# Kernel tuning notes

Measured on AMD Instinct MI355X. Metric: run time of the kernel, lower is better.

The kernel has to match this reference:

```python
import jax, jax.numpy as jnp
import numpy as np

B, D, K, N = 32, 512, 64, 1024
EPS = 1e-12  # torch F.normalize eps


def setup_inputs() -> dict:
    key = jax.random.key(0)
    k1, k2, k3 = jax.random.split(key, 3)
    x = jax.random.normal(k1, (B, D, N), dtype=jnp.float32)
    conv_w = jax.random.normal(k2, (K, D), dtype=jnp.float32) * (1.0 / np.sqrt(D))
    centers = jax.random.normal(k3, (D, K), dtype=jnp.float32)
    return {"x": x, "conv_w": conv_w, "centers": centers}


def reference(x, conv_w, centers):
    # scores: 1x1 conv over flattened spatial dim -> [B, K, N]
    scores = jnp.einsum('kd,bdn->bkn', conv_w, x)
    assign = jax.nn.softmax(scores, axis=1)                 # softmax over clusters
    # Algebraic rewrite of sum_n assign[b,k,n] * (x[b,d,n] - centers[d,k]):
    vlad = (jnp.einsum('bdn,bkn->bdk', x, assign)
            - centers[None, :, :] * assign.sum(axis=-1)[:, None, :])  # [B, D, K]
    # intra-normalization over descriptor dim D (F.normalize with eps clamp)
    vlad = vlad / jnp.maximum(jnp.linalg.norm(vlad, axis=1, keepdims=True), EPS)
    desc = vlad.reshape(vlad.shape[0], -1)                  # [B, D*K]
    desc = desc / jnp.maximum(jnp.linalg.norm(desc, axis=1, keepdims=True), EPS)
    return desc
```

## Files before the change

kernel.cpp:

```cpp
#include <hip/hip_runtime.h>
#include <hip/hip_bf16.h>

#define Bv 32
#define Dv 512
#define Kv 64
#define Nv 1024
#define EPSv 1e-12f

typedef __attribute__((ext_vector_type(8))) short bf16x8;
typedef __attribute__((ext_vector_type(4))) float f32x4;

__device__ __forceinline__ unsigned short f2b(float f) {
  union { float f; unsigned u; } v; v.f = f;
  unsigned r = v.u + 0x7fffu + ((v.u >> 16) & 1u);
  return (unsigned short)(r >> 16);
}
__device__ __forceinline__ unsigned pack2(float a, float b) {
  return (unsigned)f2b(a) | ((unsigned)f2b(b) << 16);
}

__global__ __launch_bounds__(256) void wconv(const float* __restrict__ w,
                                             unsigned short* __restrict__ wbf) {
  int i = (blockIdx.x * 256 + threadIdx.x) * 4;
  float4 v = *(const float4*)&w[i];
  uint2 o = make_uint2(pack2(v.x, v.y), pack2(v.z, v.w));
  *(uint2*)&wbf[i] = o;
}

__global__ __launch_bounds__(512) void fused_scores(
    const float* __restrict__ x, const unsigned short* __restrict__ wbf,
    unsigned short* __restrict__ xbf, unsigned short* __restrict__ assign,
    float* __restrict__ asum) {
  __shared__ unsigned short xT[64 * 520];
  __shared__ float redmax[4][64];
  __shared__ float redsum[4][64];

  const int t = threadIdx.x;
  const int b = blockIdx.y;
  const int n0 = blockIdx.x * 64;

  {
    const int lo = t & 15;
    const int hi = t >> 4;
    const float* xb = x + (size_t)b * Dv * Nv + n0;
    unsigned short* xo = xbf + (size_t)b * Dv * Nv + n0;
#pragma unroll
    for (int r = 0; r < 8; r++) {
      int d = (hi + 32 * r) * 2;
      int n4 = lo * 4;
      float4 v0 = *(const float4*)&xb[(size_t)d * Nv + n4];
      float4 v1 = *(const float4*)&xb[(size_t)(d + 1) * Nv + n4];
      *(uint2*)&xo[(size_t)d * Nv + n4] =
          make_uint2(pack2(v0.x, v0.y), pack2(v0.z, v0.w));
      *(uint2*)&xo[(size_t)(d + 1) * Nv + n4] =
          make_uint2(pack2(v1.x, v1.y), pack2(v1.z, v1.w));
      *(unsigned*)&xT[(n4 + 0) * 520 + d] = pack2(v0.x, v1.x);
      *(unsigned*)&xT[(n4 + 1) * 520 + d] = pack2(v0.y, v1.y);
      *(unsigned*)&xT[(n4 + 2) * 520 + d] = pack2(v0.z, v1.z);
      *(unsigned*)&xT[(n4 + 3) * 520 + d] = pack2(v0.w, v1.w);
    }
  }
  __syncthreads();

  const int wv = t >> 6;
  const int lane = t & 63;
  const int q = lane >> 4;
  const int m = lane & 15;
  const int k16 = wv & 3;
  const int nsub = wv >> 2;

  f32x4 acc0 = {0.f, 0.f, 0.f, 0.f};
  f32x4 acc1 = {0.f, 0.f, 0.f, 0.f};

  const unsigned short* wp = wbf + (size_t)(k16 * 16 + m) * Dv + q * 8;
  const unsigned short* l0 = &xT[(nsub * 32 + m) * 520 + q * 8];
  const unsigned short* l1 = l0 + 16 * 520;

#pragma unroll
  for (int d0 = 0; d0 < Dv; d0 += 32) {
    bf16x8 af = *(const bf16x8*)(wp + d0);
    bf16x8 bf0 = *(const bf16x8*)(l0 + d0);
    bf16x8 bf1 = *(const bf16x8*)(l1 + d0);
    acc0 = __builtin_amdgcn_mfma_f32_16x16x32_bf16(af, bf0, acc0, 0, 0, 0);
    acc1 = __builtin_amdgcn_mfma_f32_16x16x32_bf16(af, bf1, acc1, 0, 0, 0);
  }

  float m0 = fmaxf(fmaxf(acc0[0], acc0[1]), fmaxf(acc0[2], acc0[3]));
  float m1 = fmaxf(fmaxf(acc1[0], acc1[1]), fmaxf(acc1[2], acc1[3]));
  m0 = fmaxf(m0, __shfl_xor(m0, 16)); m0 = fmaxf(m0, __shfl_xor(m0, 32));
  m1 = fmaxf(m1, __shfl_xor(m1, 16)); m1 = fmaxf(m1, __shfl_xor(m1, 32));
  if (q == 0) {
    redmax[k16][nsub * 32 + m] = m0;
    redmax[k16][nsub * 32 + 16 + m] = m1;
  }
  __syncthreads();
  const int c0 = nsub * 32 + m, c1 = c0 + 16;
  float mc0 = fmaxf(fmaxf(redmax[0][c0], redmax[1][c0]), fmaxf(redmax[2][c0], redmax[3][c0]));
  float mc1 = fmaxf(fmaxf(redmax[0][c1], redmax[1][c1]), fmaxf(redmax[2][c1], redmax[3][c1]));

  float e0[4], e1[4];
  float s0 = 0.f, s1 = 0.f;
#pragma unroll
  for (int r = 0; r < 4; r++) {
    e0[r] = __expf(acc0[r] - mc0); s0 += e0[r];
    e1[r] = __expf(acc1[r] - mc1); s1 += e1[r];
  }
  s0 += __shfl_xor(s0, 16); s0 += __shfl_xor(s0, 32);
  s1 += __shfl_xor(s1, 16); s1 += __shfl_xor(s1, 32);
  if (q == 0) {
    redsum[k16][c0] = s0;
    redsum[k16][c1] = s1;
  }
  __syncthreads();
  float sc0 = 1.0f / (redsum[0][c0] + redsum[1][c0] + redsum[2][c0] + redsum[3][c0]);
  float sc1 = 1.0f / (redsum[0][c1] + redsum[1][c1] + redsum[2][c1] + redsum[3][c1]);

  unsigned short* ab = assign + ((size_t)b * Kv + k16 * 16 + q * 4) * Nv + n0 + nsub * 32;
#pragma unroll
  for (int r = 0; r < 4; r++) {
    float v0 = e0[r] * sc0;
    float v1 = e1[r] * sc1;
    ab[(size_t)r * Nv + m] = f2b(v0);
    ab[(size_t)r * Nv + 16 + m] = f2b(v1);
    float p = v0 + v1;
    p += __shfl_xor(p, 1); p += __shfl_xor(p, 2);
    p += __shfl_xor(p, 4); p += __shfl_xor(p, 8);
    if (m == 0) atomicAdd(&asum[b * Kv + k16 * 16 + q * 4 + r], p);
  }
}

__global__ __launch_bounds__(512, 4) void vlad_mfma(
    const unsigned short* __restrict__ xbf, const unsigned short* __restrict__ assign,
    const float* __restrict__ centers, const float* __restrict__ asum,
    float* __restrict__ vlad, float* __restrict__ colsq) {
  __shared__ float sred[4][64][4];

  const int t = threadIdx.x;
  const int b = blockIdx.y;
  const int d0 = blockIdx.x * 16;
  const int wv = t >> 6;
  const int ksub = wv & 3;
  const int nh = wv >> 2;
  const int lane = t & 63;
  const int q = lane >> 4;
  const int m = lane & 15;
  const int k16 = ksub * 16;

  const unsigned short* xp = xbf + ((size_t)b * Dv + d0 + m) * Nv + nh * 512 + q * 8;
  const unsigned short* ap = assign + ((size_t)b * Kv + k16 + m) * Nv + nh * 512 + q * 8;

  f32x4 acc = {0.f, 0.f, 0.f, 0.f};
  bf16x8 xv[8], av[8];
#pragma unroll
  for (int i = 0; i < 8; i++) {
    xv[i] = *(const bf16x8*)(xp + i * 32);
    av[i] = *(const bf16x8*)(ap + i * 32);
  }
#pragma unroll
  for (int i = 0; i < 8; i++) {
    acc = __builtin_amdgcn_mfma_f32_16x16x32_bf16(xv[i], av[i], acc, 0, 0, 0);
    xv[i] = *(const bf16x8*)(xp + 256 + i * 32);
    av[i] = *(const bf16x8*)(ap + 256 + i * 32);
  }
#pragma unroll
  for (int i = 0; i < 8; i++)
    acc = __builtin_amdgcn_mfma_f32_16x16x32_bf16(xv[i], av[i], acc, 0, 0, 0);

  if (nh == 1) {
#pragma unroll
    for (int r = 0; r < 4; r++) sred[ksub][lane][r] = acc[r];
  }
  __syncthreads();
  if (nh == 0) {
    const int k = k16 + m;
    const float as = asum[b * Kv + k];
    float ss = 0.f;
#pragma unroll
    for (int r = 0; r < 4; r++) {
      float v = acc[r] + sred[ksub][lane][r];
      int d = d0 + q * 4 + r;
      float val = v - centers[d * Kv + k] * as;
      vlad[((size_t)b * Dv + d) * Kv + k] = val;
      ss = fmaf(val, val, ss);
    }
    ss += __shfl_xor(ss, 16);
    ss += __shfl_xor(ss, 32);
    if (q == 0) atomicAdd(&colsq[b * Kv + k], ss);
  }
}

__global__ __launch_bounds__(256) void scale_kernel(
    const float* __restrict__ vlad, const float* __restrict__ colsq,
    float* __restrict__ out) {
  const int t = threadIdx.x;
  const size_t i = (size_t)blockIdx.x * 256 + t;
  const int b = (int)(i >> 15);
  __shared__ float scs[64];
  __shared__ float bsh;
  if (t < 64) {
    float tot = colsq[b * Kv + t];
    float sc = 1.0f / fmaxf(sqrtf(tot), EPSv);
    scs[t] = sc;
    float contrib = tot * sc * sc;
#pragma unroll
    for (int off = 32; off > 0; off >>= 1) contrib += __shfl_down(contrib, off);
    if (t == 0) bsh = 1.0f / fmaxf(sqrtf(contrib), EPSv);
  }
  __syncthreads();
  out[i] = vlad[i] * scs[i & 63] * bsh;
}

extern "C" void kernel_launch(void* const* d_in, const int* in_sizes, int n_in,
                              void* d_out, int out_size, void* d_ws, size_t ws_size,
                              hipStream_t stream) {
  const float* x = (const float*)d_in[0];
  const float* w = (const float*)d_in[1];
  const float* centers = (const float*)d_in[2];
  float* out = (float*)d_out;

  char* ws = (char*)d_ws;
  unsigned short* assign = (unsigned short*)ws;
  float* vlad = (float*)(ws + 4194304);
  unsigned short* xbf = (unsigned short*)(ws + 8388608);
  unsigned short* wbf = (unsigned short*)(ws + 41943040);
  float* asum = (float*)(ws + 42008576);
  float* colsq = asum + Bv * Kv;

  hipMemsetAsync(asum, 0, (size_t)2 * Bv * Kv * sizeof(float), stream);

  wconv<<<32, 256, 0, stream>>>(w, wbf);
  fused_scores<<<dim3(Nv / 64, Bv), 512, 0, stream>>>(x, wbf, xbf, assign, asum);
  vlad_mfma<<<dim3(Dv / 16, Bv), 512, 0, stream>>>(xbf, assign, centers, asum, vlad, colsq);
  scale_kernel<<<(Bv * Dv * Kv) / 256, 256, 0, stream>>>(vlad, colsq, out);
}
```

Before: 147.2 us.

## Drop bf16 copy of x; convert fp32 x inline in vlad GEMM

```diff
diff --git a/kernel.cpp b/kernel.cpp
--- a/kernel.cpp
+++ b/kernel.cpp
@@ -29,8 +29,7 @@
 
 __global__ __launch_bounds__(512) void fused_scores(
     const float* __restrict__ x, const unsigned short* __restrict__ wbf,
-    unsigned short* __restrict__ xbf, unsigned short* __restrict__ assign,
-    float* __restrict__ asum) {
+    unsigned short* __restrict__ assign, float* __restrict__ asum) {
   __shared__ unsigned short xT[64 * 520];
   __shared__ float redmax[4][64];
   __shared__ float redsum[4][64];
@@ -42,22 +41,26 @@
   {
     const int lo = t & 15;
     const int hi = t >> 4;
+    const int s = (lo >> 1) & 3;
     const float* xb = x + (size_t)b * Dv * Nv + n0;
-    unsigned short* xo = xbf + (size_t)b * Dv * Nv + n0;
 #pragma unroll
     for (int r = 0; r < 8; r++) {
       int d = (hi + 32 * r) * 2;
       int n4 = lo * 4;
       float4 v0 = *(const float4*)&xb[(size_t)d * Nv + n4];
       float4 v1 = *(const float4*)&xb[(size_t)(d + 1) * Nv + n4];
-      *(uint2*)&xo[(size_t)d * Nv + n4] =
-          make_uint2(pack2(v0.x, v0.y), pack2(v0.z, v0.w));
-      *(uint2*)&xo[(size_t)(d + 1) * Nv + n4] =
-          make_uint2(pack2(v1.x, v1.y), pack2(v1.z, v1.w));
-      *(unsigned*)&xT[(n4 + 0) * 520 + d] = pack2(v0.x, v1.x);
-      *(unsigned*)&xT[(n4 + 1) * 520 + d] = pack2(v0.y, v1.y);
-      *(unsigned*)&xT[(n4 + 2) * 520 + d] = pack2(v0.z, v1.z);
-      *(unsigned*)&xT[(n4 + 3) * 520 + d] = pack2(v0.w, v1.w);
+      unsigned w0 = pack2(v0.x, v1.x);
+      unsigned w1 = pack2(v0.y, v1.y);
+      unsigned w2 = pack2(v0.z, v1.z);
+      unsigned w3 = pack2(v0.w, v1.w);
+      unsigned a0 = (s & 1) ? w1 : w0, a1 = (s & 1) ? w2 : w1,
+               a2 = (s & 1) ? w3 : w2, a3 = (s & 1) ? w0 : w3;
+      unsigned b0 = (s & 2) ? a2 : a0, b1 = (s & 2) ? a3 : a1,
+               b2 = (s & 2) ? a0 : a2, b3 = (s & 2) ? a1 : a3;
+      *(unsigned*)&xT[(n4 + ((0 + s) & 3)) * 520 + d] = b0;
+      *(unsigned*)&xT[(n4 + ((1 + s) & 3)) * 520 + d] = b1;
+      *(unsigned*)&xT[(n4 + ((2 + s) & 3)) * 520 + d] = b2;
+      *(unsigned*)&xT[(n4 + ((3 + s) & 3)) * 520 + d] = b3;
     }
   }
   __syncthreads();
@@ -129,64 +132,50 @@
   }
 }
 
-__global__ __launch_bounds__(512, 4) void vlad_mfma(
-    const unsigned short* __restrict__ xbf, const unsigned short* __restrict__ assign,
+__global__ __launch_bounds__(256, 4) void vlad_mfma(
+    const float* __restrict__ x, const unsigned short* __restrict__ assign,
     const float* __restrict__ centers, const float* __restrict__ asum,
     float* __restrict__ vlad, float* __restrict__ colsq) {
-  __shared__ float sred[4][64][4];
-
   const int t = threadIdx.x;
   const int b = blockIdx.y;
   const int d0 = blockIdx.x * 16;
-  const int wv = t >> 6;
-  const int ksub = wv & 3;
-  const int nh = wv >> 2;
+  const int ksub = t >> 6;
   const int lane = t & 63;
   const int q = lane >> 4;
   const int m = lane & 15;
   const int k16 = ksub * 16;
 
-  const unsigned short* xp = xbf + ((size_t)b * Dv + d0 + m) * Nv + nh * 512 + q * 8;
-  const unsigned short* ap = assign + ((size_t)b * Kv + k16 + m) * Nv + nh * 512 + q * 8;
+  const float* xp = x + ((size_t)b * Dv + d0 + m) * Nv + q * 8;
+  const unsigned short* ap = assign + ((size_t)b * Kv + k16 + m) * Nv + q * 8;
 
   f32x4 acc = {0.f, 0.f, 0.f, 0.f};
-  bf16x8 xv[8], av[8];
-#pragma unroll
-  for (int i = 0; i < 8; i++) {
-    xv[i] = *(const bf16x8*)(xp + i * 32);
-    av[i] = *(const bf16x8*)(ap + i * 32);
-  }
-#pragma unroll
-  for (int i = 0; i < 8; i++) {
-    acc = __builtin_amdgcn_mfma_f32_16x16x32_bf16(xv[i], av[i], acc, 0, 0, 0);
-    xv[i] = *(const bf16x8*)(xp + 256 + i * 32);
-    av[i] = *(const bf16x8*)(ap + 256 + i * 32);
-  }
-#pragma unroll
-  for (int i = 0; i < 8; i++)
-    acc = __builtin_amdgcn_mfma_f32_16x16x32_bf16(xv[i], av[i], acc, 0, 0, 0);
-
-  if (nh == 1) {
-#pragma unroll
-    for (int r = 0; r < 4; r++) sred[ksub][lane][r] = acc[r];
-  }
-  __syncthreads();
-  if (nh == 0) {
-    const int k = k16 + m;
-    const float as = asum[b * Kv + k];
-    float ss = 0.f;
-#pragma unroll
-    for (int r = 0; r < 4; r++) {
-      float v = acc[r] + sred[ksub][lane][r];
-      int d = d0 + q * 4 + r;
-      float val = v - centers[d * Kv + k] * as;
-      vlad[((size_t)b * Dv + d) * Kv + k] = val;
-      ss = fmaf(val, val, ss);
-    }
-    ss += __shfl_xor(ss, 16);
-    ss += __shfl_xor(ss, 32);
-    if (q == 0) atomicAdd(&colsq[b * Kv + k], ss);
-  }
+#pragma unroll
+  for (int n = 0; n < Nv; n += 32) {
+    float4 f0 = *(const float4*)(xp + n);
+    float4 f1 = *(const float4*)(xp + n + 4);
+    bf16x8 av = *(const bf16x8*)(ap + n);
+    bf16x8 xv;
+    unsigned* xu = (unsigned*)&xv;
+    xu[0] = pack2(f0.x, f0.y);
+    xu[1] = pack2(f0.z, f0.w);
+    xu[2] = pack2(f1.x, f1.y);
+    xu[3] = pack2(f1.z, f1.w);
+    acc = __builtin_amdgcn_mfma_f32_16x16x32_bf16(xv, av, acc, 0, 0, 0);
+  }
+
+  const int k = k16 + m;
+  const float as = asum[b * Kv + k];
+  float ss = 0.f;
+#pragma unroll
+  for (int r = 0; r < 4; r++) {
+    int d = d0 + q * 4 + r;
+    float val = acc[r] - centers[d * Kv + k] * as;
+    vlad[((size_t)b * Dv + d) * Kv + k] = val;
+    ss = fmaf(val, val, ss);
+  }
+  ss += __shfl_xor(ss, 16);
+  ss += __shfl_xor(ss, 32);
+  if (q == 0) atomicAdd(&colsq[b * Kv + k], ss);
 }
 
 __global__ __launch_bounds__(256) void scale_kernel(
@@ -221,15 +210,14 @@
   char* ws = (char*)d_ws;
   unsigned short* assign = (unsigned short*)ws;
   float* vlad = (float*)(ws + 4194304);
-  unsigned short* xbf = (unsigned short*)(ws + 8388608);
-  unsigned short* wbf = (unsigned short*)(ws + 41943040);
-  float* asum = (float*)(ws + 42008576);
+  unsigned short* wbf = (unsigned short*)(ws + 8388608);
+  float* asum = (float*)(ws + 8454144);
   float* colsq = asum + Bv * Kv;
 
   hipMemsetAsync(asum, 0, (size_t)2 * Bv * Kv * sizeof(float), stream);
 
   wconv<<<32, 256, 0, stream>>>(w, wbf);
-  fused_scores<<<dim3(Nv / 64, Bv), 512, 0, stream>>>(x, wbf, xbf, assign, asum);
-  vlad_mfma<<<dim3(Dv / 16, Bv), 512, 0, stream>>>(xbf, assign, centers, asum, vlad, colsq);
+  fused_scores<<<dim3(Nv / 64, Bv), 512, 0, stream>>>(x, wbf, assign, asum);
+  vlad_mfma<<<dim3(Dv / 16, Bv), 256, 0, stream>>>(x, assign, centers, asum, vlad, colsq);
   scale_kernel<<<(Bv * Dv * Kv) / 256, 256, 0, stream>>>(vlad, colsq, out);
 }
```

New measurement: 154.8 us. 5.2% more time.

## Tile xbf and assign by 64-column blocks and swizzle LDS transpose writes

Applied to the files above, without the earlier changes.

```diff
diff --git a/kernel.cpp b/kernel.cpp
--- a/kernel.cpp
+++ b/kernel.cpp
@@ -37,27 +37,37 @@
 
   const int t = threadIdx.x;
   const int b = blockIdx.y;
-  const int n0 = blockIdx.x * 64;
+  const int nt = blockIdx.x;
+  const int n0 = nt * 64;
 
   {
     const int lo = t & 15;
     const int hi = t >> 4;
+    const int s = (lo >> 1) & 3;
     const float* xb = x + (size_t)b * Dv * Nv + n0;
-    unsigned short* xo = xbf + (size_t)b * Dv * Nv + n0;
+    unsigned short* xt = xbf + ((size_t)b * 16 + nt) * (Dv * 64);
 #pragma unroll
     for (int r = 0; r < 8; r++) {
       int d = (hi + 32 * r) * 2;
       int n4 = lo * 4;
       float4 v0 = *(const float4*)&xb[(size_t)d * Nv + n4];
       float4 v1 = *(const float4*)&xb[(size_t)(d + 1) * Nv + n4];
-      *(uint2*)&xo[(size_t)d * Nv + n4] =
+      *(uint2*)&xt[(size_t)d * 64 + n4] =
           make_uint2(pack2(v0.x, v0.y), pack2(v0.z, v0.w));
-      *(uint2*)&xo[(size_t)(d + 1) * Nv + n4] =
+      *(uint2*)&xt[(size_t)(d + 1) * 64 + n4] =
           make_uint2(pack2(v1.x, v1.y), pack2(v1.z, v1.w));
-      *(unsigned*)&xT[(n4 + 0) * 520 + d] = pack2(v0.x, v1.x);
-      *(unsigned*)&xT[(n4 + 1) * 520 + d] = pack2(v0.y, v1.y);
-      *(unsigned*)&xT[(n4 + 2) * 520 + d] = pack2(v0.z, v1.z);
-      *(unsigned*)&xT[(n4 + 3) * 520 + d] = pack2(v0.w, v1.w);
+      unsigned w0 = pack2(v0.x, v1.x);
+      unsigned w1 = pack2(v0.y, v1.y);
+      unsigned w2 = pack2(v0.z, v1.z);
+      unsigned w3 = pack2(v0.w, v1.w);
+      unsigned a0 = (s & 1) ? w1 : w0, a1 = (s & 1) ? w2 : w1,
+               a2 = (s & 1) ? w3 : w2, a3 = (s & 1) ? w0 : w3;
+      unsigned b0 = (s & 2) ? a2 : a0, b1 = (s & 2) ? a3 : a1,
+               b2 = (s & 2) ? a0 : a2, b3 = (s & 2) ? a1 : a3;
+      *(unsigned*)&xT[(n4 + ((0 + s) & 3)) * 520 + d] = b0;
+      *(unsigned*)&xT[(n4 + ((1 + s) & 3)) * 520 + d] = b1;
+      *(unsigned*)&xT[(n4 + ((2 + s) & 3)) * 520 + d] = b2;
+      *(unsigned*)&xT[(n4 + ((3 + s) & 3)) * 520 + d] = b3;
     }
   }
   __syncthreads();
@@ -115,13 +125,14 @@
   float sc0 = 1.0f / (redsum[0][c0] + redsum[1][c0] + redsum[2][c0] + redsum[3][c0]);
   float sc1 = 1.0f / (redsum[0][c1] + redsum[1][c1] + redsum[2][c1] + redsum[3][c1]);
 
-  unsigned short* ab = assign + ((size_t)b * Kv + k16 * 16 + q * 4) * Nv + n0 + nsub * 32;
+  unsigned short* at_ = assign + ((size_t)b * 16 + nt) * (Kv * 64)
+                        + (size_t)(k16 * 16 + q * 4) * 64 + nsub * 32;
 #pragma unroll
   for (int r = 0; r < 4; r++) {
     float v0 = e0[r] * sc0;
     float v1 = e1[r] * sc1;
-    ab[(size_t)r * Nv + m] = f2b(v0);
-    ab[(size_t)r * Nv + 16 + m] = f2b(v1);
+    at_[r * 64 + m] = f2b(v0);
+    at_[r * 64 + 16 + m] = f2b(v1);
     float p = v0 + v1;
     p += __shfl_xor(p, 1); p += __shfl_xor(p, 2);
     p += __shfl_xor(p, 4); p += __shfl_xor(p, 8);
@@ -129,7 +140,7 @@
   }
 }
 
-__global__ __launch_bounds__(512, 4) void vlad_mfma(
+__global__ __launch_bounds__(512, 2) void vlad_mfma(
     const unsigned short* __restrict__ xbf, const unsigned short* __restrict__ assign,
     const float* __restrict__ centers, const float* __restrict__ asum,
     float* __restrict__ vlad, float* __restrict__ colsq) {
@@ -146,22 +157,29 @@
   const int m = lane & 15;
   const int k16 = ksub * 16;
 
-  const unsigned short* xp = xbf + ((size_t)b * Dv + d0 + m) * Nv + nh * 512 + q * 8;
-  const unsigned short* ap = assign + ((size_t)b * Kv + k16 + m) * Nv + nh * 512 + q * 8;
+  const unsigned short* xp = xbf + ((size_t)b * 16 + nh * 8) * (Dv * 64)
+                             + (size_t)(d0 + m) * 64 + q * 8;
+  const unsigned short* ap = assign + ((size_t)b * 16 + nh * 8) * (Kv * 64)
+                             + (size_t)(k16 + m) * 64 + q * 8;
 
   f32x4 acc = {0.f, 0.f, 0.f, 0.f};
   bf16x8 xv[8], av[8];
+
 #pragma unroll
   for (int i = 0; i < 8; i++) {
-    xv[i] = *(const bf16x8*)(xp + i * 32);
-    av[i] = *(const bf16x8*)(ap + i * 32);
-  }
+    xv[i] = *(const bf16x8*)(xp + (i >> 1) * (Dv * 64) + (i & 1) * 32);
+    av[i] = *(const bf16x8*)(ap + (i >> 1) * (Kv * 64) + (i & 1) * 32);
+  }
+  __builtin_amdgcn_sched_barrier(0);
+
 #pragma unroll
   for (int i = 0; i < 8; i++) {
     acc = __builtin_amdgcn_mfma_f32_16x16x32_bf16(xv[i], av[i], acc, 0, 0, 0);
-    xv[i] = *(const bf16x8*)(xp + 256 + i * 32);
-    av[i] = *(const bf16x8*)(ap + 256 + i * 32);
-  }
+    xv[i] = *(const bf16x8*)(xp + ((i + 8) >> 1) * (Dv * 64) + (i & 1) * 32);
+    av[i] = *(const bf16x8*)(ap + ((i + 8) >> 1) * (Kv * 64) + (i & 1) * 32);
+    __builtin_amdgcn_sched_barrier(0);
+  }
+
 #pragma unroll
   for (int i = 0; i < 8; i++)
     acc = __builtin_amdgcn_mfma_f32_16x16x32_bf16(xv[i], av[i], acc, 0, 0, 0);
```

After: 145.3 us. About the same (-1.3%).
